# Optimization experiments

Measured on AMD Instinct MI355X. Metric: run time of the kernel, lower is better.

The kernel has to match this reference:

```python
import jax, jax.numpy as jnp
import numpy as np

MARGIN = 0.2


def setup_inputs() -> dict:
    key = jax.random.key(0)
    k1, k2 = jax.random.split(key)
    B, D, C = 4096, 512, 512
    embeddings = jax.random.normal(k1, (B, D), dtype=jnp.float32)
    labels = jax.random.randint(k2, (B,), 0, C, dtype=jnp.int64)
    return {"embeddings": embeddings, "labels": labels}


def reference(embeddings, labels):
    B = embeddings.shape[0]
    # L2-normalize rows (eps matches torch F.normalize default 1e-12)
    norm = jnp.maximum(jnp.linalg.norm(embeddings, axis=1, keepdims=True), 1e-12)
    e = embeddings / norm
    # cosine distance matrix [B, B]
    dist = 1.0 - e @ e.T
    same = labels[:, None] == labels[None, :]
    eye = jnp.eye(B, dtype=bool)
    pos_mask = same & ~eye
    neg_mask = ~same
    # dist in [0, 2]; sentinels outside that range for masked reductions
    hardest_pos = jnp.max(jnp.where(pos_mask, dist, -1.0), axis=1)
    hardest_neg = jnp.min(jnp.where(neg_mask, dist, 3.0), axis=1)
    valid = jnp.any(pos_mask, axis=1) & jnp.any(neg_mask, axis=1)
    per_anchor = jax.nn.relu(hardest_pos - hardest_neg + MARGIN)
    loss_sum = jnp.sum(jnp.where(valid, per_anchor, 0.0))
    n_valid = jnp.maximum(jnp.sum(valid.astype(jnp.int32)), 1)
    return loss_sum / n_valid.astype(embeddings.dtype)
```

## Files before the change

### kernel.cpp

```cpp
#include <hip/hip_runtime.h>
#include <hip/hip_bf16.h>

#define BDIM 4096
#define DDIM 512
#define BT 128
#define BK 32
#define NKT (DDIM / BK)
#define NPAN (BDIM / BT)
#define NTRI (NPAN * (NPAN + 1) / 2)

typedef __bf16 bf16x8 __attribute__((ext_vector_type(8)));
typedef float f32x4 __attribute__((ext_vector_type(4)));
typedef unsigned short ushort_t;

__device__ inline ushort_t f2bf(float f) {
  __hip_bfloat16 h = __float2bfloat16(f);
  return *reinterpret_cast<ushort_t*>(&h);
}

__device__ inline unsigned int enc_f32(float x) {
  unsigned int u = __float_as_uint(x);
  return (u & 0x80000000u) ? ~u : (u | 0x80000000u);
}
__device__ inline float dec_f32(unsigned int e) {
  unsigned int u = (e & 0x80000000u) ? (e ^ 0x80000000u) : ~e;
  return __uint_as_float(u);
}

__global__ __launch_bounds__(256) void norm_kernel(const float* __restrict__ x,
                                                   ushort_t* __restrict__ e,
                                                   unsigned int* __restrict__ minpos_e,
                                                   unsigned int* __restrict__ maxneg_e) {
  if (blockIdx.x == 0) {
    const unsigned int init_min = enc_f32(1e30f);
    const unsigned int init_max = enc_f32(-1e30f);
    for (int i = threadIdx.x; i < BDIM; i += 256) {
      minpos_e[i] = init_min;
      maxneg_e[i] = init_max;
    }
  }
  const int row  = blockIdx.x * 4 + (threadIdx.x >> 6);
  const int lane = threadIdx.x & 63;
  const float4* xr = reinterpret_cast<const float4*>(x + (size_t)row * DDIM);
  float4 v0 = xr[lane];
  float4 v1 = xr[lane + 64];
  float ss = v0.x*v0.x + v0.y*v0.y + v0.z*v0.z + v0.w*v0.w
           + v1.x*v1.x + v1.y*v1.y + v1.z*v1.z + v1.w*v1.w;
#pragma unroll
  for (int off = 32; off >= 1; off >>= 1) ss += __shfl_xor(ss, off);
  const float inv = 1.0f / fmaxf(sqrtf(ss), 1e-12f);

  ushort4 p0, p1;
  p0.x = f2bf(v0.x * inv); p0.y = f2bf(v0.y * inv);
  p0.z = f2bf(v0.z * inv); p0.w = f2bf(v0.w * inv);
  p1.x = f2bf(v1.x * inv); p1.y = f2bf(v1.y * inv);
  p1.z = f2bf(v1.z * inv); p1.w = f2bf(v1.w * inv);
  ushort4* er = reinterpret_cast<ushort4*>(e + (size_t)row * DDIM);
  er[lane]      = p0;
  er[lane + 64] = p1;
}

#define STAGE(buf, kt)                                                         \
  do {                                                                         \
    _Pragma("unroll")                                                          \
    for (int q = 0; q < 4; ++q) {                                              \
      if (q >= 2 && diag) continue;            \
      const int off  = q * 4096 + tid * 16;                      \
      const int loff = off & 8191;                                             \
      const int row  = loff >> 6;                                              \
      const int kb   = loff & 63;                                              \
      const int pan  = (q < 2) ? Ibase : Jbase;                                \
      const char* src = (const char*)e + (size_t)(pan + row) * (DDIM * 2) +    \
                        (kt) * 64 + kb;                                        \
      __builtin_amdgcn_global_load_lds(                                        \
          (const __attribute__((address_space(1))) void*)src,                  \
          (__attribute__((address_space(3))) void*)(&Blds[buf][off]),          \
          16, 0, 0);                                                           \
    }                                                                          \
  } while (0)

__global__ __launch_bounds__(256, 4) void gemm_reduce_kernel(
    const ushort_t* __restrict__ e, const int* __restrict__ labels,
    unsigned int* __restrict__ minpos_e, unsigned int* __restrict__ maxneg_e) {
  __shared__ __align__(16) char Blds[2][16384];
  __shared__ int Llab[256];

  const int tid  = threadIdx.x;
  const int wave = tid >> 6;
  const int lane = tid & 63;
  const int l15  = lane & 15;
  const int g    = lane >> 4;
  const int wr   = wave >> 1;
  const int wc   = wave & 1;

  const int bid = blockIdx.x;
  const int t   = (bid & 7) * (NTRI / 8) + (bid >> 3);
  int I = (int)((65.0f - sqrtf(4225.0f - 8.0f * (float)t)) * 0.5f);
  while (32 * (I + 1) - ((I + 1) * I) / 2 <= t) ++I;
  while (32 * I - (I * (I - 1)) / 2 > t) --I;
  const int J = I + (t - (32 * I - (I * (I - 1)) / 2));
  const int Ibase = I * BT;
  const int Jbase = J * BT;
  const bool diag = (I == J);

  if (tid < 128) Llab[tid] = labels[Ibase + tid];
  else           Llab[tid] = labels[Jbase + tid - 128];

  f32x4 acc[4][4];
#pragma unroll
  for (int m = 0; m < 4; ++m)
#pragma unroll
    for (int n = 0; n < 4; ++n) acc[m][n] = (f32x4){0.f, 0.f, 0.f, 0.f};

  STAGE(0, 0);
  __syncthreads();

  const int bofs = diag ? 0 : 8192;
  for (int kt = 0; kt < NKT; ++kt) {
    if (kt + 1 < NKT) STAGE((kt + 1) & 1, kt + 1);

    const char* Ab = Blds[kt & 1];
    const char* Bb = Blds[kt & 1] + bofs;
    bf16x8 a[4], b[4];
#pragma unroll
    for (int m = 0; m < 4; ++m)
      a[m] = *reinterpret_cast<const bf16x8*>(
          Ab + (wr * 64 + m * 16 + l15) * 64 + g * 16);
#pragma unroll
    for (int n = 0; n < 4; ++n)
      b[n] = *reinterpret_cast<const bf16x8*>(
          Bb + (wc * 64 + n * 16 + l15) * 64 + g * 16);
#pragma unroll
    for (int m = 0; m < 4; ++m)
#pragma unroll
      for (int n = 0; n < 4; ++n)
        acc[m][n] = __builtin_amdgcn_mfma_f32_16x16x32_bf16(a[m], b[n],
                                                            acc[m][n], 0, 0, 0);
    __syncthreads();
  }

  float cmp[4], cmx[4];
  int lj[4], gj[4];
#pragma unroll
  for (int n = 0; n < 4; ++n) {
    cmp[n] = 1e30f; cmx[n] = -1e30f;
    gj[n]  = Jbase + wc * 64 + n * 16 + l15;
    lj[n]  = Llab[128 + wc * 64 + n * 16 + l15];
  }
  float rmp[4][4], rmx[4][4];
#pragma unroll
  for (int m = 0; m < 4; ++m)
#pragma unroll
    for (int r = 0; r < 4; ++r) { rmp[m][r] = 1e30f; rmx[m][r] = -1e30f; }

#pragma unroll
  for (int m = 0; m < 4; ++m) {
#pragma unroll
    for (int r = 0; r < 4; ++r) {
      const int rloc = wr * 64 + m * 16 + g * 4 + r;
      const int li   = Llab[rloc];
      const int gi   = Ibase + rloc;
#pragma unroll
      for (int n = 0; n < 4; ++n) {
        const float v = acc[m][n][r];
        if (li == lj[n]) {
          if (gi != gj[n]) {
            rmp[m][r] = fminf(rmp[m][r], v);
            cmp[n]    = fminf(cmp[n], v);
          }
        } else {
          rmx[m][r] = fmaxf(rmx[m][r], v);
          cmx[n]    = fmaxf(cmx[n], v);
        }
      }
    }
  }

#pragma unroll
  for (int off = 16; off <= 32; off <<= 1) {
#pragma unroll
    for (int n = 0; n < 4; ++n) {
      cmp[n] = fminf(cmp[n], __shfl_xor(cmp[n], off));
      cmx[n] = fmaxf(cmx[n], __shfl_xor(cmx[n], off));
    }
  }
#pragma unroll
  for (int off = 1; off < 16; off <<= 1) {
#pragma unroll
    for (int m = 0; m < 4; ++m)
#pragma unroll
      for (int r = 0; r < 4; ++r) {
        rmp[m][r] = fminf(rmp[m][r], __shfl_xor(rmp[m][r], off));
        rmx[m][r] = fmaxf(rmx[m][r], __shfl_xor(rmx[m][r], off));
      }
  }

  if (g == 0) {
#pragma unroll
    for (int n = 0; n < 4; ++n) {
      if (cmp[n] < 1e29f)  atomicMin(&minpos_e[gj[n]], enc_f32(cmp[n]));
      if (cmx[n] > -1e29f) atomicMax(&maxneg_e[gj[n]], enc_f32(cmx[n]));
    }
  }
  if (l15 == 0) {
#pragma unroll
    for (int m = 0; m < 4; ++m)
#pragma unroll
      for (int r = 0; r < 4; ++r) {
        const int gi = Ibase + wr * 64 + m * 16 + g * 4 + r;
        if (rmp[m][r] < 1e29f)  atomicMin(&minpos_e[gi], enc_f32(rmp[m][r]));
        if (rmx[m][r] > -1e29f) atomicMax(&maxneg_e[gi], enc_f32(rmx[m][r]));
      }
  }
}

__global__ __launch_bounds__(1024) void finalize_kernel(
    const unsigned int* __restrict__ minpos_e, const unsigned int* __restrict__ maxneg_e,
    float* __restrict__ out) {
  const int tid = threadIdx.x;
  float sum = 0.f;
  int cnt = 0;
  for (int row = tid; row < BDIM; row += 1024) {
    const float mp = dec_f32(minpos_e[row]);
    const float mn = dec_f32(maxneg_e[row]);
    if (mp < 1e29f && mn > -1e29f) {
      sum += fmaxf(0.f, mn - mp + 0.2f);
      cnt += 1;
    }
  }
#pragma unroll
  for (int off = 32; off >= 1; off >>= 1) {
    sum += __shfl_xor(sum, off);
    cnt += __shfl_xor(cnt, off);
  }
  __shared__ float wsum[16];
  __shared__ int   wcnt[16];
  const int wv = tid >> 6, ln = tid & 63;
  if (ln == 0) { wsum[wv] = sum; wcnt[wv] = cnt; }
  __syncthreads();
  if (tid == 0) {
    float S = 0.f; int C = 0;
    for (int w = 0; w < 16; ++w) { S += wsum[w]; C += wcnt[w]; }
    out[0] = S / (float)(C > 0 ? C : 1);
  }
}

extern "C" void kernel_launch(void* const* d_in, const int* in_sizes, int n_in,
                              void* d_out, int out_size, void* d_ws, size_t ws_size,
                              hipStream_t stream) {
  const float* x      = (const float*)d_in[0];
  const int*   labels = (const int*)d_in[1];
  float* out = (float*)d_out;

  char* ws = (char*)d_ws;
  ushort_t* e            = (ushort_t*)ws;
  unsigned int* minpos_e = (unsigned int*)(ws + (size_t)BDIM * DDIM * 2);
  unsigned int* maxneg_e = minpos_e + BDIM;

  norm_kernel<<<BDIM / 4, 256, 0, stream>>>(x, e, minpos_e, maxneg_e);
  gemm_reduce_kernel<<<NTRI, 256, 0, stream>>>(e, labels, minpos_e, maxneg_e);
  finalize_kernel<<<1, 1024, 0, stream>>>(minpos_e, maxneg_e, out);
}
```

Baseline: 36.68 us.

## Pre-swizzle embeddings into MFMA fragment layout, drop LDS, fuse finalize

The norm kernel now writes normalized bf16 embeddings in a blocked layout that matches the MFMA operand fragments. This lets the GEMM load operands straight from global memory into registers with no LDS staging or barriers. The GEMM moves to single-wave blocks with 64x64 triangular tiles, so there are many more blocks, and it software-pipelines loads with double register buffers. The finalize kernel is removed: the last block to finish, found through an atomic counter, computes the loss. In exchange, operands are reloaded from L2 with less reuse per block and there are more label and atomic operations.

Measured after the change: 87.53 us. +138.6%, slower.

```diff
diff --git a/kernel.cpp b/kernel.cpp
--- a/kernel.cpp
+++ b/kernel.cpp
@@ -3,11 +3,10 @@
 
 #define BDIM 4096
 #define DDIM 512
-#define BT 128
-#define BK 32
-#define NKT (DDIM / BK)
-#define NPAN (BDIM / BT)
-#define NTRI (NPAN * (NPAN + 1) / 2)
+#define TS 64
+#define NT (BDIM / TS)
+#define NTRI (NT * (NT + 1) / 2)
+#define NKT (DDIM / 32)
 
 typedef __bf16 bf16x8 __attribute__((ext_vector_type(8)));
 typedef float f32x4 __attribute__((ext_vector_type(4)));
@@ -30,7 +29,8 @@
 __global__ __launch_bounds__(256) void norm_kernel(const float* __restrict__ x,
                                                    ushort_t* __restrict__ e,
                                                    unsigned int* __restrict__ minpos_e,
-                                                   unsigned int* __restrict__ maxneg_e) {
+                                                   unsigned int* __restrict__ maxneg_e,
+                                                   unsigned int* __restrict__ done_ctr) {
   if (blockIdx.x == 0) {
     const unsigned int init_min = enc_f32(1e30f);
     const unsigned int init_max = enc_f32(-1e30f);
@@ -38,6 +38,7 @@
       minpos_e[i] = init_min;
       maxneg_e[i] = init_max;
     }
+    if (threadIdx.x == 0) done_ctr[0] = 0u;
   }
   const int row  = blockIdx.x * 4 + (threadIdx.x >> 6);
   const int lane = threadIdx.x & 63;
@@ -55,97 +56,83 @@
   p0.z = f2bf(v0.z * inv); p0.w = f2bf(v0.w * inv);
   p1.x = f2bf(v1.x * inv); p1.y = f2bf(v1.y * inv);
   p1.z = f2bf(v1.z * inv); p1.w = f2bf(v1.w * inv);
-  ushort4* er = reinterpret_cast<ushort4*>(e + (size_t)row * DDIM);
-  er[lane]      = p0;
-  er[lane + 64] = p1;
-}
-
-#define STAGE(buf, kt)                                                         \
+
+  const int rb = row >> 4, ir = row & 15;
+  const int kc = lane >> 1;
+  const int ke = (lane & 1) * 4;
+  ushort_t* base = e + ((size_t)rb * 64) * 128 + ir * 8 + ke;
+  *reinterpret_cast<ushort4*>(base + (size_t)kc * 128)        = p0;
+  *reinterpret_cast<ushort4*>(base + (size_t)(32 + kc) * 128) = p1;
+}
+
+__global__ __launch_bounds__(64, 2) void gemm_reduce_kernel(
+    const ushort_t* __restrict__ e, const int* __restrict__ labels,
+    unsigned int* __restrict__ minpos_e, unsigned int* __restrict__ maxneg_e,
+    unsigned int* __restrict__ done_ctr, float* __restrict__ out) {
+  const int lane = threadIdx.x;
+  const int l15  = lane & 15;
+  const int g    = lane >> 4;
+
+  const int bid = blockIdx.x;
+  const int t   = (bid & 7) * (NTRI / 8) + (bid >> 3);
+  int I = (int)(64.5f - sqrtf(4160.25f - 2.0f * (float)t));
+  if (I < 0) I = 0;
+  if (I > NT - 1) I = NT - 1;
+  while (I < NT - 1 && 64 * (I + 1) - ((I + 1) * I) / 2 <= t) ++I;
+  while (I > 0 && 64 * I - (I * (I - 1)) / 2 > t) --I;
+  const int J = I + (t - (64 * I - (I * (I - 1)) / 2));
+
+  const ushort_t* baseA = e + ((size_t)(4 * I) * 64) * 128 + lane * 8;
+  const ushort_t* baseB = e + ((size_t)(4 * J) * 64) * 128 + lane * 8;
+
+  f32x4 acc[4][4];
+#pragma unroll
+  for (int m = 0; m < 4; ++m)
+#pragma unroll
+    for (int n = 0; n < 4; ++n) acc[m][n] = (f32x4){0.f, 0.f, 0.f, 0.f};
+
+#define LOADF(av, bv, kt)                                                      \
   do {                                                                         \
     _Pragma("unroll")                                                          \
-    for (int q = 0; q < 4; ++q) {                                              \
-      if (q >= 2 && diag) continue;            \
-      const int off  = q * 4096 + tid * 16;                      \
-      const int loff = off & 8191;                                             \
-      const int row  = loff >> 6;                                              \
-      const int kb   = loff & 63;                                              \
-      const int pan  = (q < 2) ? Ibase : Jbase;                                \
-      const char* src = (const char*)e + (size_t)(pan + row) * (DDIM * 2) +    \
-                        (kt) * 64 + kb;                                        \
-      __builtin_amdgcn_global_load_lds(                                        \
-          (const __attribute__((address_space(1))) void*)src,                  \
-          (__attribute__((address_space(3))) void*)(&Blds[buf][off]),          \
-          16, 0, 0);                                                           \
+    for (int m = 0; m < 4; ++m) {                                              \
+      av[m] = *reinterpret_cast<const bf16x8*>(baseA + m * 8192 + (kt) * 512); \
+      bv[m] = *reinterpret_cast<const bf16x8*>(baseB + m * 8192 + (kt) * 512); \
     }                                                                          \
   } while (0)
 
-__global__ __launch_bounds__(256, 4) void gemm_reduce_kernel(
-    const ushort_t* __restrict__ e, const int* __restrict__ labels,
-    unsigned int* __restrict__ minpos_e, unsigned int* __restrict__ maxneg_e) {
-  __shared__ __align__(16) char Blds[2][16384];
-  __shared__ int Llab[256];
-
-  const int tid  = threadIdx.x;
-  const int wave = tid >> 6;
-  const int lane = tid & 63;
-  const int l15  = lane & 15;
-  const int g    = lane >> 4;
-  const int wr   = wave >> 1;
-  const int wc   = wave & 1;
-
-  const int bid = blockIdx.x;
-  const int t   = (bid & 7) * (NTRI / 8) + (bid >> 3);
-  int I = (int)((65.0f - sqrtf(4225.0f - 8.0f * (float)t)) * 0.5f);
-  while (32 * (I + 1) - ((I + 1) * I) / 2 <= t) ++I;
-  while (32 * I - (I * (I - 1)) / 2 > t) --I;
-  const int J = I + (t - (32 * I - (I * (I - 1)) / 2));
-  const int Ibase = I * BT;
-  const int Jbase = J * BT;
-  const bool diag = (I == J);
-
-  if (tid < 128) Llab[tid] = labels[Ibase + tid];
-  else           Llab[tid] = labels[Jbase + tid - 128];
-
-  f32x4 acc[4][4];
-#pragma unroll
-  for (int m = 0; m < 4; ++m)
-#pragma unroll
-    for (int n = 0; n < 4; ++n) acc[m][n] = (f32x4){0.f, 0.f, 0.f, 0.f};
-
-  STAGE(0, 0);
-  __syncthreads();
-
-  const int bofs = diag ? 0 : 8192;
-  for (int kt = 0; kt < NKT; ++kt) {
-    if (kt + 1 < NKT) STAGE((kt + 1) & 1, kt + 1);
-
-    const char* Ab = Blds[kt & 1];
-    const char* Bb = Blds[kt & 1] + bofs;
-    bf16x8 a[4], b[4];
-#pragma unroll
-    for (int m = 0; m < 4; ++m)
-      a[m] = *reinterpret_cast<const bf16x8*>(
-          Ab + (wr * 64 + m * 16 + l15) * 64 + g * 16);
-#pragma unroll
-    for (int n = 0; n < 4; ++n)
-      b[n] = *reinterpret_cast<const bf16x8*>(
-          Bb + (wc * 64 + n * 16 + l15) * 64 + g * 16);
-#pragma unroll
-    for (int m = 0; m < 4; ++m)
-#pragma unroll
-      for (int n = 0; n < 4; ++n)
-        acc[m][n] = __builtin_amdgcn_mfma_f32_16x16x32_bf16(a[m], b[n],
-                                                            acc[m][n], 0, 0, 0);
-    __syncthreads();
-  }
+#define MF(av, bv)                                                             \
+  do {                                                                         \
+    _Pragma("unroll")                                                          \
+    for (int m = 0; m < 4; ++m)                                                \
+      _Pragma("unroll")                                                        \
+      for (int n = 0; n < 4; ++n)                                              \
+        acc[m][n] = __builtin_amdgcn_mfma_f32_16x16x32_bf16(av[m], bv[n],      \
+                                                            acc[m][n], 0, 0, 0);\
+  } while (0)
+
+  bf16x8 aA[4], bA[4], aB[4], bB[4];
+  LOADF(aA, bA, 0);
+  LOADF(aB, bB, 1);
+#pragma unroll
+  for (int kt = 0; kt < NKT; kt += 2) {
+    MF(aA, bA);
+    if (kt + 2 < NKT) LOADF(aA, bA, kt + 2);
+    MF(aB, bB);
+    if (kt + 3 < NKT) LOADF(aB, bB, kt + 3);
+  }
+#undef LOADF
+#undef MF
+
+  const int lab_i = labels[I * TS + lane];
+  const int lab_j = labels[J * TS + lane];
 
   float cmp[4], cmx[4];
   int lj[4], gj[4];
 #pragma unroll
   for (int n = 0; n < 4; ++n) {
     cmp[n] = 1e30f; cmx[n] = -1e30f;
-    gj[n]  = Jbase + wc * 64 + n * 16 + l15;
-    lj[n]  = Llab[128 + wc * 64 + n * 16 + l15];
+    gj[n]  = J * TS + n * 16 + l15;
+    lj[n]  = __shfl(lab_j, n * 16 + l15);
   }
   float rmp[4][4], rmx[4][4];
 #pragma unroll
@@ -157,9 +144,8 @@
   for (int m = 0; m < 4; ++m) {
 #pragma unroll
     for (int r = 0; r < 4; ++r) {
-      const int rloc = wr * 64 + m * 16 + g * 4 + r;
-      const int li   = Llab[rloc];
-      const int gi   = Ibase + rloc;
+      const int gi = I * TS + m * 16 + g * 4 + r;
+      const int li = __shfl(lab_i, m * 16 + g * 4 + r);
 #pragma unroll
       for (int n = 0; n < 4; ++n) {
         const float v = acc[m][n][r];
@@ -207,41 +193,38 @@
     for (int m = 0; m < 4; ++m)
 #pragma unroll
       for (int r = 0; r < 4; ++r) {
-        const int gi = Ibase + wr * 64 + m * 16 + g * 4 + r;
+        const int gi = I * TS + m * 16 + g * 4 + r;
         if (rmp[m][r] < 1e29f)  atomicMin(&minpos_e[gi], enc_f32(rmp[m][r]));
         if (rmx[m][r] > -1e29f) atomicMax(&maxneg_e[gi], enc_f32(rmx[m][r]));
       }
   }
-}
-
-__global__ __launch_bounds__(1024) void finalize_kernel(
-    const unsigned int* __restrict__ minpos_e, const unsigned int* __restrict__ maxneg_e,
-    float* __restrict__ out) {
-  const int tid = threadIdx.x;
-  float sum = 0.f;
-  int cnt = 0;
-  for (int row = tid; row < BDIM; row += 1024) {
-    const float mp = dec_f32(minpos_e[row]);
-    const float mn = dec_f32(maxneg_e[row]);
-    if (mp < 1e29f && mn > -1e29f) {
-      sum += fmaxf(0.f, mn - mp + 0.2f);
-      cnt += 1;
-    }
-  }
-#pragma unroll
-  for (int off = 32; off >= 1; off >>= 1) {
-    sum += __shfl_xor(sum, off);
-    cnt += __shfl_xor(cnt, off);
-  }
-  __shared__ float wsum[16];
-  __shared__ int   wcnt[16];
-  const int wv = tid >> 6, ln = tid & 63;
-  if (ln == 0) { wsum[wv] = sum; wcnt[wv] = cnt; }
-  __syncthreads();
-  if (tid == 0) {
-    float S = 0.f; int C = 0;
-    for (int w = 0; w < 16; ++w) { S += wsum[w]; C += wcnt[w]; }
-    out[0] = S / (float)(C > 0 ? C : 1);
+
+  __threadfence();
+  unsigned int rank = 0;
+  if (lane == 0) rank = atomicAdd(done_ctr, 1u);
+  rank = __shfl(rank, 0);
+  if (rank == NTRI - 1) {
+    __threadfence();
+    float sum = 0.f;
+    int cnt = 0;
+    for (int row = lane; row < BDIM; row += 64) {
+      const unsigned int ump = __hip_atomic_load(&minpos_e[row], __ATOMIC_RELAXED,
+                                                 __HIP_MEMORY_SCOPE_AGENT);
+      const unsigned int umn = __hip_atomic_load(&maxneg_e[row], __ATOMIC_RELAXED,
+                                                 __HIP_MEMORY_SCOPE_AGENT);
+      const float mp = dec_f32(ump);
+      const float mn = dec_f32(umn);
+      if (mp < 1e29f && mn > -1e29f) {
+        sum += fmaxf(0.f, mn - mp + 0.2f);
+        cnt += 1;
+      }
+    }
+#pragma unroll
+    for (int off = 32; off >= 1; off >>= 1) {
+      sum += __shfl_xor(sum, off);
+      cnt += __shfl_xor(cnt, off);
+    }
+    if (lane == 0) out[0] = sum / (float)(cnt > 0 ? cnt : 1);
   }
 }
 
@@ -256,8 +239,9 @@
   ushort_t* e            = (ushort_t*)ws;
   unsigned int* minpos_e = (unsigned int*)(ws + (size_t)BDIM * DDIM * 2);
   unsigned int* maxneg_e = minpos_e + BDIM;
-
-  norm_kernel<<<BDIM / 4, 256, 0, stream>>>(x, e, minpos_e, maxneg_e);
-  gemm_reduce_kernel<<<NTRI, 256, 0, stream>>>(e, labels, minpos_e, maxneg_e);
-  finalize_kernel<<<1, 1024, 0, stream>>>(minpos_e, maxneg_e, out);
-}
+  unsigned int* done_ctr = maxneg_e + BDIM;
+
+  norm_kernel<<<BDIM / 4, 256, 0, stream>>>(x, e, minpos_e, maxneg_e, done_ctr);
+  gemm_reduce_kernel<<<NTRI, 64, 0, stream>>>(e, labels, minpos_e, maxneg_e,
+                                              done_ctr, out);
+}
```
